# Optimization experiments

Measured on AMD Instinct MI355X. Metric: run time of the kernel, lower is better.

## Reference

```python
import jax, jax.numpy as jnp
import numpy as np

B, N, H, DK, DV = 2, 2048, 16, 128, 128
E = H * DV
EPS = 1e-6


def setup_inputs() -> dict:
    key = jax.random.key(0)
    ks = jax.random.split(key, 8)
    sc_qk = 1.0 / np.sqrt(E + H * DK)  # xavier_normal-ish std
    sc_e = 1.0 / np.sqrt(2 * E)
    d = {
        "x": jax.random.normal(ks[0], (B, N, E), jnp.float32),
        "Wq": jax.random.normal(ks[1], (H * DK, E), jnp.float32) * sc_qk,
        "bq": jnp.zeros((H * DK,), jnp.float32),
        "Wk": jax.random.normal(ks[2], (H * DK, E), jnp.float32) * sc_qk,
        "bk": jnp.zeros((H * DK,), jnp.float32),
        "Wv": jax.random.normal(ks[3], (E, E), jnp.float32) * sc_e,
        "bv": jnp.zeros((E,), jnp.float32),
        "Wg": jax.random.normal(ks[4], (E, E), jnp.float32) * sc_e,
        "bg": jnp.zeros((E,), jnp.float32),
        "Wo": jax.random.normal(ks[5], (E, E), jnp.float32) * sc_e,
        "bo": jnp.zeros((E,), jnp.float32),
        "start_idx": 0,
    }
    return d


def _retention_scan(q, k, v, decays):
    # q,k: [B,N,H,DK] (k already scaled), v: [B,N,H,DV]
    qs = jnp.moveaxis(q, 1, 0)  # [N,B,H,DK]
    ks_ = jnp.moveaxis(k, 1, 0)
    vs = jnp.moveaxis(v, 1, 0)
    dec = decays[None, :, None, None]  # [1,H,1,1]

    def step(state, qkv):
        qt, kt, vt = qkv
        # state_n = decay * state_{n-1} + k_n (x) v_n
        state = dec * state + kt[..., :, None] * vt[..., None, :]  # [B,H,DK,DV]
        ret = jnp.einsum("bhk,bhkv->bhv", qt, state)
        return state, ret

    init = jnp.zeros((q.shape[0], H, DK, DV), q.dtype)
    final_state, rets = jax.lax.scan(step, init, (qs, ks_, vs))
    return jnp.moveaxis(rets, 0, 1), final_state  # [B,N,H,DV], [B,H,DK,DV]


def reference(x, Wq, bq, Wk, bk, Wv, bv, Wg, bg, Wo, bo, start_idx):
    b, n, _ = x.shape
    decays = 1.0 - jnp.exp2(-5.0 - jnp.arange(H, dtype=jnp.float32))  # [H]
    q = (x @ Wq.T + bq).reshape(b, n, H, DK)
    k = (x @ Wk.T + bk).reshape(b, n, H, DK) / (DK ** 0.5)
    v = (x @ Wv.T + bv).reshape(b, n, H, DV)
    retention, state = _retention_scan(q, k, v, decays)
    # GroupNorm over (b n) tokens, num_groups=H, channels=E, no affine
    r = retention.reshape(b * n, H, DV).astype(jnp.float32)
    mu = jnp.mean(r, axis=-1, keepdims=True)
    var = jnp.var(r, axis=-1, keepdims=True)
    r = (r - mu) / jnp.sqrt(var + EPS)
    r = r.reshape(b, n, E).astype(x.dtype)
    gate = jax.nn.silu(x @ Wg.T + bg)
    out = (r * gate) @ Wo.T + bo
    return out, state
```

## Files before the change

kernel.cpp:

```cpp
#include <hip/hip_runtime.h>
#include <hip/hip_bf16.h>

typedef __attribute__((ext_vector_type(8))) short short8;
typedef __attribute__((ext_vector_type(4))) short short4v;
typedef __attribute__((ext_vector_type(4))) float floatx4;

#define DI __device__ __forceinline__

constexpr int B_ = 2, N_ = 2048, H_ = 16, DK_ = 128, DV_ = 128, E_ = 2048;
constexpr int M_ = B_ * N_;
constexpr int NCAT_ = 4 * E_;
constexpr int CH_ = 128;
constexpr int NC_ = N_ / CH_;
constexpr float KSCALE = 0.08838834764831845f;

constexpr long OFF_XB   = 0;
constexpr long OFF_WCAT = 16777216;
constexpr long OFF_WOB  = 50331648;
constexpr long OFF_BCAT = 58720256;
constexpr long OFF_Y    = 58753024;
constexpr long OFF_KT   = 125861888;
constexpr long OFF_VT   = 142639104;
constexpr long OFF_SCB  = 159416320;

DI unsigned short f2bf(float f){
  unsigned u = __float_as_uint(f);
  u += 0x7fffu + ((u >> 16) & 1u);
  return (unsigned short)(u >> 16);
}
DI float bf2f(unsigned short s){ return __uint_as_float(((unsigned)s) << 16); }

DI void gload_lds16(const void* g, void* l){
  __builtin_amdgcn_global_load_lds(
      (const __attribute__((address_space(1))) unsigned int*)g,
      (__attribute__((address_space(3))) unsigned int*)l, 16, 0, 0);
}

__global__ void k_cast(const float* __restrict__ s, unsigned short* __restrict__ d, int n){
  long i = ((long)blockIdx.x * blockDim.x + threadIdx.x) * 8;
  if(i >= n) return;
  float4 v0 = *(const float4*)(s + i);
  float4 v1 = *(const float4*)(s + i + 4);
  short8 o;
  o[0]=(short)f2bf(v0.x); o[1]=(short)f2bf(v0.y); o[2]=(short)f2bf(v0.z); o[3]=(short)f2bf(v0.w);
  o[4]=(short)f2bf(v1.x); o[5]=(short)f2bf(v1.y); o[6]=(short)f2bf(v1.z); o[7]=(short)f2bf(v1.w);
  *(short8*)(d + i) = o;
}

__global__ void k_bcat(const float* __restrict__ bq, const float* __restrict__ bk,
                       const float* __restrict__ bv, const float* __restrict__ bg,
                       float* __restrict__ bcat){
  int i = blockIdx.x * blockDim.x + threadIdx.x;
  float v;
  if(i < 2048)      v = bq[i];
  else if(i < 4096) v = bk[i - 2048];
  else if(i < 6144) v = bv[i - 4096];
  else              v = bg[i - 6144];
  bcat[i] = v;
}

__global__ __launch_bounds__(512, 2)
void k_gemm256(const unsigned short* __restrict__ A,
               const unsigned short* __restrict__ Bt,
               unsigned short* __restrict__ Y,
               const float* __restrict__ bias)
{
  extern __shared__ unsigned short lds[];
  constexpr int K = 2048;
  constexpr int NKT = K / 64;

  const int tid = threadIdx.x;
  const int wave = tid >> 6, lane = tid & 63;
  const int wr = wave >> 2, wc = wave & 3;
  const int l15 = lane & 15;

  int bid = blockIdx.x;
  int g = bid & 7, w = bid >> 3;
  int bm = (g & 1) * 8 + (w & 7);
  int bn = (g >> 1) * 8 + (w >> 3);

  const unsigned short* Ab = A  + (long)bm * 256 * K;
  const unsigned short* Bb = Bt + (long)bn * 256 * K;

  const int srow = wave * 8 + (lane >> 3);
  const int ce   = ((lane & 7) ^ ((lane >> 3) & 7)) * 8;

  const int colb[2] = { (((lane >> 4)    ) ^ (lane & 7)) << 4,
                        (((lane >> 4) + 4 ^ (lane & 7))) << 4 };
  int rbA[4], rbB[2];
  #pragma unroll
  for(int i=0;i<4;++i) rbA[i] = (wr*64 + i*16 + l15) << 7;
  #pragma unroll
  for(int j=0;j<2;++j) rbB[j] = (wc*32 + j*16 + l15) << 7;

  floatx4 acc[4][4][2] = {};
  short8 ar[4][2], br[2][2];
  const char* ldsc = (const char*)lds;

#define STG(op, buf, half, kt) do{                                                   \
    const unsigned short* _s = ((op) ? Bb : Ab) + (long)((half)*128 + srow)*K + (long)(kt)*64 + ce; \
    unsigned short* _d = lds + ((op)*32768 + (buf)*16384 + (half)*8192 + wave*512);  \
    gload_lds16(_s, _d);                                                             \
    gload_lds16(_s + 64*K, _d + 4096);                                               \
  }while(0)

#define RD_A(buf, half) do{                                                          \
    const char* _h = ldsc + (buf)*32768 + (half)*16384;                              \
    _Pragma("unroll")                                                                \
    for(int i=0;i<4;++i){ ar[i][0] = *(const short8*)(_h + rbA[i] + colb[0]);        \
                          ar[i][1] = *(const short8*)(_h + rbA[i] + colb[1]); }      \
  }while(0)

#define RD_B(buf, half) do{                                                          \
    const char* _h = ldsc + 65536 + (buf)*32768 + (half)*16384;                      \
    _Pragma("unroll")                                                                \
    for(int j=0;j<2;++j){ br[j][0] = *(const short8*)(_h + rbB[j] + colb[0]);        \
                          br[j][1] = *(const short8*)(_h + rbB[j] + colb[1]); }      \
  }while(0)

#define MFMA16(q) do{                                                                \
    __builtin_amdgcn_s_setprio(1);                                                   \
    _Pragma("unroll")                                                                \
    for(int i=0;i<4;++i)                                                             \
      _Pragma("unroll")                                                              \
      for(int j=0;j<2;++j)                                                           \
        _Pragma("unroll")                                                            \
        for(int k=0;k<2;++k)                                                         \
          acc[q][i][j] = __builtin_amdgcn_mfma_f32_16x16x32_bf16(ar[i][k], br[j][k], acc[q][i][j], 0,0,0); \
    __builtin_amdgcn_s_setprio(0);                                                   \
  }while(0)

  STG(0, 0, 0, 0);
  STG(1, 0, 0, 0);
  STG(1, 0, 1, 0);
  STG(0, 0, 1, 0);
  asm volatile("s_waitcnt vmcnt(0)" ::: "memory");
  __builtin_amdgcn_s_barrier();
  __builtin_amdgcn_sched_barrier(0);

  for(int u=0; u<NKT; ++u){
    const int cur = u & 1, nxt = cur ^ 1;
    const int ktn = (u + 1) & (NKT - 1);

    RD_A(cur, 0);
    RD_B(cur, 0);
    STG(0, nxt, 0, ktn);
    asm volatile("s_waitcnt vmcnt(4)" ::: "memory");
    __builtin_amdgcn_s_barrier();
    MFMA16(0);
    __builtin_amdgcn_s_barrier();
    __builtin_amdgcn_sched_barrier(0);

    RD_B(cur, 1);
    STG(1, nxt, 0, ktn);
    asm volatile("s_waitcnt vmcnt(4)" ::: "memory");
    __builtin_amdgcn_s_barrier();
    MFMA16(1);
    __builtin_amdgcn_s_barrier();
    __builtin_amdgcn_sched_barrier(0);

    RD_A(cur, 1);
    STG(1, nxt, 1, ktn);
    __builtin_amdgcn_s_barrier();
    MFMA16(2);
    __builtin_amdgcn_s_barrier();
    __builtin_amdgcn_sched_barrier(0);

    RD_B(cur, 0);
    STG(0, nxt, 1, ktn);
    asm volatile("s_waitcnt vmcnt(4)" ::: "memory");
    __builtin_amdgcn_s_barrier();
    MFMA16(3);
    __builtin_amdgcn_s_barrier();
    __builtin_amdgcn_sched_barrier(0);
  }
#undef STG
#undef RD_A
#undef RD_B
#undef MFMA16

  static constexpr int QM[4] = {0,0,1,1}, QN[4] = {0,1,1,0};
  #pragma unroll
  for(int q=0;q<4;++q){
    #pragma unroll
    for(int i=0;i<4;++i){
      const int rowi = bm*256 + QM[q]*128 + wr*64 + i*16 + ((lane>>4)<<2);
      #pragma unroll
      for(int j=0;j<2;++j){
        const int col = bn*256 + QN[q]*128 + wc*32 + j*16 + l15;
        const float bs = bias[col];
        const int sec = col >> 11;
        #pragma unroll
        for(int r=0;r<4;++r){
          float v = acc[q][i][j][r] + bs;
          if(sec == 1) v *= KSCALE;
          else if(sec == 3) v = v / (1.f + __expf(-v));
          Y[(long)(rowi + r) * NCAT_ + col] = f2bf(v);
        }
      }
    }
  }
}

template<int EPI>
__global__ __launch_bounds__(256)
void k_gemm(const unsigned short* __restrict__ A,
            const unsigned short* __restrict__ Bt,
            void* __restrict__ outp,
            const float* __restrict__ bias,
            int M, int Ncols, int K, int NB)
{
  __shared__ unsigned short lA[128*64];
  __shared__ unsigned short lB[128*64];
  const int bid = blockIdx.x;
  const int bm = bid / NB, bn = bid % NB;
  const int tid = threadIdx.x;
  const int wave = tid >> 6, lane = tid & 63;
  const int wr = wave >> 1, wc = wave & 1;

  floatx4 acc[4][4] = {};

  int srow[4], scol[4];
  #pragma unroll
  for(int is=0; is<4; ++is){
    int o = is*4096 + wave*1024 + lane*16;
    int row = o >> 7;
    int logcb = (o & 127) ^ ((row & 7) << 4);
    srow[is] = row; scol[is] = logcb >> 1;
  }
  const unsigned short* Abase = A + (long)bm * 128 * K;
  const unsigned short* Bbase = Bt + (long)bn * 128 * K;

  const int nkt = K >> 6;
  for(int kt=0; kt<nkt; ++kt){
    const int k0 = kt << 6;
    #pragma unroll
    for(int is=0; is<4; ++is){
      gload_lds16(Abase + (long)srow[is]*K + k0 + scol[is], &lA[(is*4096 + wave*1024) >> 1]);
      gload_lds16(Bbase + (long)srow[is]*K + k0 + scol[is], &lB[(is*4096 + wave*1024) >> 1]);
    }
    __syncthreads();
    #pragma unroll
    for(int kk=0; kk<2; ++kk){
      const int cb = (kk<<6) + ((lane>>4)<<4);
      short8 af[4], bfr[4];
      #pragma unroll
      for(int i=0;i<4;++i){
        int row = (wr<<6) + (i<<4) + (lane&15);
        af[i] = *(const short8*)((const char*)lA + (row<<7) + (cb ^ ((row&7)<<4)));
      }
      #pragma unroll
      for(int j=0;j<4;++j){
        int row = (wc<<6) + (j<<4) + (lane&15);
        bfr[j] = *(const short8*)((const char*)lB + (row<<7) + (cb ^ ((row&7)<<4)));
      }
      #pragma unroll
      for(int i=0;i<4;++i)
        #pragma unroll
        for(int j=0;j<4;++j)
          acc[i][j] = __builtin_amdgcn_mfma_f32_16x16x32_bf16(af[i], bfr[j], acc[i][j], 0,0,0);
    }
    __syncthreads();
  }

  #pragma unroll
  for(int i=0;i<4;++i){
    #pragma unroll
    for(int j=0;j<4;++j){
      #pragma unroll
      for(int r=0;r<4;++r){
        int row = bm*128 + (wr<<6) + (i<<4) + ((lane>>4)<<2) + r;
        int col = bn*128 + (wc<<6) + (j<<4) + (lane&15);
        float v = acc[i][j][r] + bias[col];
        if(EPI == 0){
          int sec = col >> 11;
          if(sec == 1) v *= KSCALE;
          else if(sec == 3) v = v / (1.f + __expf(-v));
          ((unsigned short*)outp)[(long)row * Ncols + col] = f2bf(v);
        } else {
          ((float*)outp)[(long)row * Ncols + col] = v;
        }
      }
    }
  }
}

__global__ __launch_bounds__(256)
void k_transpose(const unsigned short* __restrict__ Y,
                 unsigned short* __restrict__ Kt, unsigned short* __restrict__ Vt){
  __shared__ unsigned short lt[128][136];
  int bid = blockIdx.x;
  int op = bid >> 9;
  int r  = bid & 511;
  int bh = r >> 4, c = r & 15, b = bh >> 4, h = bh & 15;
  int tid = threadIdx.x;
  float dec = 1.f - exp2f(-5.f - (float)h);
  float l2d = log2f(dec);
  int sec = op ? 4096 : 2048;
  unsigned short* Dst = op ? Vt : Kt;

  #pragma unroll
  for(int p=0;p<8;++p){
    int t = p*16 + (tid>>4);
    long src = ((long)(b*N_ + c*CH_ + t)) * NCAT_ + sec + h*128 + (tid&15)*8;
    short8 v = *(const short8*)(Y + src);
    if(op == 0){
      float f = exp2f(-(float)t * l2d);
      #pragma unroll
      for(int u=0;u<8;++u) v[u] = (short)f2bf(bf2f((unsigned short)v[u]) * f);
    }
    *(short8*)&lt[t][(tid&15)*8] = v;
  }
  __syncthreads();
  #pragma unroll
  for(int p=0;p<8;++p){
    int dk = p*16 + (tid>>4);
    int tc = (tid&15)*8;
    short8 o;
    #pragma unroll
    for(int u=0;u<8;++u) o[u] = (short)lt[tc+u][dk];
    *(short8*)(Dst + ((long)(bh*128 + dk)) * N_ + c*CH_ + tc) = o;
  }
}

__global__ __launch_bounds__(256)
void k_chunksum(const unsigned short* __restrict__ Ktd, const unsigned short* __restrict__ Vt,
                float* __restrict__ MS){
  int bid = blockIdx.x;
  int bh = bid >> 4, c = bid & 15, h = bh & 15;
  int tid = threadIdx.x, wave = tid >> 6, lane = tid & 63;
  int wr = wave >> 1, wc = wave & 1;
  floatx4 acc[4][4] = {};
  const unsigned short* Vb = Vt  + (long)bh*128*N_ + c*CH_;
  const unsigned short* Kb = Ktd + (long)bh*128*N_ + c*CH_;

  #pragma unroll
  for(int kk=0;kk<4;++kk){
    int tl = kk*32 + ((lane>>4)<<3);
    short8 af[4], bfr[4];
    #pragma unroll
    for(int i=0;i<4;++i){ int dv = (wr<<6)+(i<<4)+(lane&15); af[i]  = *(const short8*)(Vb + (long)dv*N_ + tl); }
    #pragma unroll
    for(int j=0;j<4;++j){ int dk = (wc<<6)+(j<<4)+(lane&15); bfr[j] = *(const short8*)(Kb + (long)dk*N_ + tl); }
    #pragma unroll
    for(int i=0;i<4;++i)
      #pragma unroll
      for(int j=0;j<4;++j)
        acc[i][j] = __builtin_amdgcn_mfma_f32_16x16x32_bf16(af[i], bfr[j], acc[i][j], 0,0,0);
  }
  float dec = 1.f - exp2f(-5.f - (float)h);
  float scale = exp2f(127.f * log2f(dec));
  float* Mo = MS + ((long)bh*NC_ + c) * 16384;
  #pragma unroll
  for(int i=0;i<4;++i)
    #pragma unroll
    for(int j=0;j<4;++j)
      #pragma unroll
      for(int r=0;r<4;++r){
        int dv = (wr<<6)+(i<<4)+((lane>>4)<<2)+r;
        int dk = (wc<<6)+(j<<4)+(lane&15);
        Mo[dv*128 + dk] = acc[i][j][r] * scale;
      }
}

__global__ __launch_bounds__(256)
void k_scan(const float* __restrict__ MS, unsigned short* __restrict__ Scb,
            float* __restrict__ stateOut){
  int bid = blockIdx.x;
  int bh = bid >> 4, p = bid & 15;
  int tid = threadIdx.x, h = bh & 15;
  float dec = 1.f - exp2f(-5.f - (float)h);
  float decC = exp2f(128.f * log2f(dec));
  int e0 = p*1024 + tid*4;
  floatx4 S = {0.f, 0.f, 0.f, 0.f};
  const float* base = MS + (long)bh * NC_ * 16384 + e0;
  unsigned short* sb = Scb + (long)bh * NC_ * 16384 + e0;
  for(int c=0;c<NC_;++c){
    floatx4 m = *(const floatx4*)(base + (long)c*16384);
    short4v q;
    #pragma unroll
    for(int u=0;u<4;++u) q[u] = (short)f2bf(S[u]);
    *(short4v*)(sb + (long)c*16384) = q;
    S = decC * S + m;
  }
  int dv = e0 >> 7, dk = e0 & 127;
  float* so = stateOut + (long)bh*16384 + dv;
  #pragma unroll
  for(int u=0;u<4;++u) so[(long)(dk+u)*128] = S[u];
}

__global__ __launch_bounds__(256)
void k_ret(const unsigned short* __restrict__ Y, const unsigned short* __restrict__ Vt,
           const unsigned short* __restrict__ Scb, unsigned short* __restrict__ RG){
  __shared__ unsigned short sQ[128*128];
  __shared__ unsigned short sK[128*128];
  int bid = blockIdx.x;
  int bh = bid >> 4, c = bid & 15, b = bh >> 4, h = bh & 15;
  int tid = threadIdx.x, w = tid >> 6, lane = tid & 63;
  float dec = 1.f - exp2f(-5.f - (float)h);
  float l2d = log2f(dec);

  #pragma unroll
  for(int p=0;p<8;++p){
    int t = p*16 + (tid>>4);
    long row = (long)(b*N_ + c*CH_ + t) * NCAT_ + h*128 + (tid&15)*8;
    short8 qv = *(const short8*)(Y + row);
    short8 kv = *(const short8*)(Y + row + 2048);
    float fq = exp2f((float)t * l2d);
    float fk = exp2f(-(float)t * l2d);
    short8 qs, ks;
    #pragma unroll
    for(int u=0;u<8;++u){
      qs[u] = (short)f2bf(bf2f((unsigned short)qv[u]) * fq);
      ks[u] = (short)f2bf(bf2f((unsigned short)kv[u]) * fk);
    }
    int ad = t*256 + (((tid&15)*16) ^ ((t&7)<<4));
    *(short8*)((char*)sQ + ad) = qs;
    *(short8*)((char*)sK + ad) = ks;
  }
  __syncthreads();

  floatx4 acc[2][8] = {};
  #pragma unroll
  for(int kk=0;kk<4;++kk){
    int cb = (kk<<6) + ((lane>>4)<<4);
    short8 af[2], bfr[8];
    #pragma unroll
    for(int i=0;i<2;++i){ int t = w*32 + (i<<4) + (lane&15); af[i] = *(const short8*)((const char*)sQ + t*256 + (cb ^ ((t&7)<<4))); }
    #pragma unroll
    for(int j=0;j<8;++j){ int s = (j<<4) + (lane&15); bfr[j] = *(const short8*)((const char*)sK + s*256 + (cb ^ ((s&7)<<4))); }
    #pragma unroll
    for(int i=0;i<2;++i)
      #pragma unroll
      for(int j=0;j<8;++j)
        acc[i][j] = __builtin_amdgcn_mfma_f32_16x16x32_bf16(af[i], bfr[j], acc[i][j], 0,0,0);
  }
  __syncthreads();

  #pragma unroll
  for(int i=0;i<2;++i)
    #pragma unroll
    for(int j=0;j<8;++j)
      #pragma unroll
      for(int r=0;r<4;++r){
        int t = w*32 + (i<<4) + ((lane>>4)<<2) + r;
        int s = (j<<4) + (lane&15);
        float v = (s <= t) ? acc[i][j][r] : 0.f;
        *(unsigned short*)((char*)sK + t*256 + ((s*2) ^ ((t&7)<<4))) = f2bf(v);
      }
  __syncthreads();

  #pragma unroll
  for(int i=0;i<2;++i)
    #pragma unroll
    for(int j=0;j<8;++j)
      #pragma unroll
      for(int u=0;u<4;++u) acc[i][j][u] = 0.f;

  const unsigned short* Vb = Vt + (long)bh*128*N_ + c*CH_;
  #pragma unroll
  for(int kk=0;kk<4;++kk){
    int cb = (kk<<6) + ((lane>>4)<<4);
    int sg = kk*32 + ((lane>>4)<<3);
    short8 af[2], bfr[8];
    #pragma unroll
    for(int i=0;i<2;++i){ int t = w*32 + (i<<4) + (lane&15); af[i] = *(const short8*)((const char*)sK + t*256 + (cb ^ ((t&7)<<4))); }
    #pragma unroll
    for(int j=0;j<8;++j){ int dv = (j<<4) + (lane&15); bfr[j] = *(const short8*)(Vb + (long)dv*N_ + sg); }
    #pragma unroll
    for(int i=0;i<2;++i)
      #pragma unroll
      for(int j=0;j<8;++j)
        acc[i][j] = __builtin_amdgcn_mfma_f32_16x16x32_bf16(af[i], bfr[j], acc[i][j], 0,0,0);
  }
  const unsigned short* Sb = Scb + ((long)bh*NC_ + c) * 16384;
  #pragma unroll
  for(int kk=0;kk<4;++kk){
    int cb = (kk<<6) + ((lane>>4)<<4);
    int kg = kk*32 + ((lane>>4)<<3);
    short8 af[2], bfr[8];
    #pragma unroll
    for(int i=0;i<2;++i){
      int t = w*32 + (i<<4) + (lane&15);
      short8 qv = *(const short8*)((const char*)sQ + t*256 + (cb ^ ((t&7)<<4)));
      #pragma unroll
      for(int u=0;u<8;++u) af[i][u] = (short)f2bf(bf2f((unsigned short)qv[u]) * dec);
    }
    #pragma unroll
    for(int j=0;j<8;++j){ int dv = (j<<4) + (lane&15); bfr[j] = *(const short8*)(Sb + (long)dv*128 + kg); }
    #pragma unroll
    for(int i=0;i<2;++i)
      #pragma unroll
      for(int j=0;j<8;++j)
        acc[i][j] = __builtin_amdgcn_mfma_f32_16x16x32_bf16(af[i], bfr[j], acc[i][j], 0,0,0);
  }

  #pragma unroll
  for(int i=0;i<2;++i){
    #pragma unroll
    for(int r=0;r<4;++r){
      float s1 = 0.f, s2 = 0.f;
      #pragma unroll
      for(int j=0;j<8;++j){ float v = acc[i][j][r]; s1 += v; s2 += v*v; }
      #pragma unroll
      for(int off=1; off<16; off<<=1){ s1 += __shfl_xor(s1, off); s2 += __shfl_xor(s2, off); }
      float mu  = s1 * (1.f/128.f);
      float var = s2 * (1.f/128.f) - mu*mu;
      float inv = rsqrtf(var + 1e-6f);
      int t = w*32 + (i<<4) + ((lane>>4)<<2) + r;
      long mrow = (long)(b*N_ + c*CH_ + t);
      #pragma unroll
      for(int j=0;j<8;++j){
        int dv = (j<<4) + (lane&15);
        float v = (acc[i][j][r] - mu) * inv;
        float g = bf2f(Y[mrow*NCAT_ + 6144 + h*128 + dv]);
        RG[mrow*E_ + h*128 + dv] = f2bf(v * g);
      }
    }
  }
}

extern "C" void kernel_launch(void* const* d_in, const int* in_sizes, int n_in,
                              void* d_out, int out_size, void* d_ws, size_t ws_size,
                              hipStream_t stream) {
  const float* x  = (const float*)d_in[0];
  const float* Wq = (const float*)d_in[1];
  const float* bq = (const float*)d_in[2];
  const float* Wk = (const float*)d_in[3];
  const float* bk = (const float*)d_in[4];
  const float* Wv = (const float*)d_in[5];
  const float* bv = (const float*)d_in[6];
  const float* Wg = (const float*)d_in[7];
  const float* bg = (const float*)d_in[8];
  const float* Wo = (const float*)d_in[9];
  const float* bo = (const float*)d_in[10];

  char* ws = (char*)d_ws;
  unsigned short* xb   = (unsigned short*)(ws + OFF_XB);
  unsigned short* Wcat = (unsigned short*)(ws + OFF_WCAT);
  unsigned short* Wob  = (unsigned short*)(ws + OFF_WOB);
  float*          bcat = (float*)(ws + OFF_BCAT);
  unsigned short* Y    = (unsigned short*)(ws + OFF_Y);
  unsigned short* Ktd  = (unsigned short*)(ws + OFF_KT);
  unsigned short* Vt   = (unsigned short*)(ws + OFF_VT);
  unsigned short* Scb  = (unsigned short*)(ws + OFF_SCB);
  float*          MS   = (float*)(ws + OFF_WCAT);
  unsigned short* RG   = (unsigned short*)(ws + OFF_XB);

  float* outp     = (float*)d_out;
  float* stateOut = outp + (long)M_ * E_;

  (void)hipFuncSetAttribute((const void*)k_gemm256,
                            hipFuncAttributeMaxDynamicSharedMemorySize, 131072);

  k_cast<<<4096, 256, 0, stream>>>(x, xb, M_*E_);
  k_cast<<<2048, 256, 0, stream>>>(Wq, Wcat + 0L,        E_*E_);
  k_cast<<<2048, 256, 0, stream>>>(Wk, Wcat + 1L*E_*E_,  E_*E_);
  k_cast<<<2048, 256, 0, stream>>>(Wv, Wcat + 2L*E_*E_,  E_*E_);
  k_cast<<<2048, 256, 0, stream>>>(Wg, Wcat + 3L*E_*E_,  E_*E_);
  k_cast<<<2048, 256, 0, stream>>>(Wo, Wob, E_*E_);
  k_bcat<<<32, 256, 0, stream>>>(bq, bk, bv, bg, bcat);

  k_gemm256<<<512, 512, 131072, stream>>>(xb, Wcat, Y, bcat);

  k_transpose<<<1024, 256, 0, stream>>>(Y, Ktd, Vt);

  k_chunksum<<<512, 256, 0, stream>>>(Ktd, Vt, MS);
  k_scan<<<512, 256, 0, stream>>>(MS, Scb, stateOut);
  k_ret<<<512, 256, 0, stream>>>(Y, Vt, Scb, RG);

  k_gemm<1><<<(M_/128)*(E_/128), 256, 0, stream>>>(RG, Wob, (void*)outp, bo, M_, E_, E_, E_/128);
}
```

Before: 295.3 us.

## Simplify fused projection GEMM pipeline and double-buffer the output GEMM

The 256x256-tile projection GEMM drops its hand-scheduled four-phase loop, which used partial vmcnt waits, barriers and priority hints. In its place is a plain double-buffered loop: one __syncthreads, prefetch of the next K-tile into the other buffer, then two k-steps of 8x4 MFMAs over the whole tile. The 128x128 output GEMM gets a second LDS buffer so the next tile's global-to-LDS loads overlap the current tile's MFMAs, which also removes one barrier per iteration. The trade is simpler code and more overlap in the small GEMM, at the risk of less fine-grained memory/compute interleaving in the large GEMM. The doubled LDS use in the small GEMM may also lower occupancy.

```diff
diff --git a/kernel.cpp b/kernel.cpp
--- a/kernel.cpp
+++ b/kernel.cpp
@@ -85,16 +85,15 @@
   const int srow = wave * 8 + (lane >> 3);
   const int ce   = ((lane & 7) ^ ((lane >> 3) & 7)) * 8;
 
-  const int colb[2] = { (((lane >> 4)    ) ^ (lane & 7)) << 4,
-                        (((lane >> 4) + 4 ^ (lane & 7))) << 4 };
-  int rbA[4], rbB[2];
-  #pragma unroll
-  for(int i=0;i<4;++i) rbA[i] = (wr*64 + i*16 + l15) << 7;
-  #pragma unroll
-  for(int j=0;j<2;++j) rbB[j] = (wc*32 + j*16 + l15) << 7;
-
-  floatx4 acc[4][4][2] = {};
-  short8 ar[4][2], br[2][2];
+  const int colb[2] = { ((((lane >> 4))    ^ (lane & 7)) << 4),
+                        ((((lane >> 4)+4)  ^ (lane & 7)) << 4) };
+  int rbA[8], rbB[4];
+  #pragma unroll
+  for(int ai=0;ai<8;++ai) rbA[ai] = (ai>>2)*16384 + ((wr*64 + (ai&3)*16 + l15) << 7);
+  #pragma unroll
+  for(int bj=0;bj<4;++bj) rbB[bj] = (bj>>1)*16384 + ((wc*32 + (bj&1)*16 + l15) << 7);
+
+  floatx4 acc[8][4] = {};
   const char* ldsc = (const char*)lds;
 
 #define STG(op, buf, half, kt) do{                                                   \
@@ -104,99 +103,55 @@
     gload_lds16(_s + 64*K, _d + 4096);                                               \
   }while(0)
 
-#define RD_A(buf, half) do{                                                          \
-    const char* _h = ldsc + (buf)*32768 + (half)*16384;                              \
-    _Pragma("unroll")                                                                \
-    for(int i=0;i<4;++i){ ar[i][0] = *(const short8*)(_h + rbA[i] + colb[0]);        \
-                          ar[i][1] = *(const short8*)(_h + rbA[i] + colb[1]); }      \
-  }while(0)
-
-#define RD_B(buf, half) do{                                                          \
-    const char* _h = ldsc + 65536 + (buf)*32768 + (half)*16384;                      \
-    _Pragma("unroll")                                                                \
-    for(int j=0;j<2;++j){ br[j][0] = *(const short8*)(_h + rbB[j] + colb[0]);        \
-                          br[j][1] = *(const short8*)(_h + rbB[j] + colb[1]); }      \
-  }while(0)
-
-#define MFMA16(q) do{                                                                \
-    __builtin_amdgcn_s_setprio(1);                                                   \
-    _Pragma("unroll")                                                                \
-    for(int i=0;i<4;++i)                                                             \
-      _Pragma("unroll")                                                              \
-      for(int j=0;j<2;++j)                                                           \
-        _Pragma("unroll")                                                            \
-        for(int k=0;k<2;++k)                                                         \
-          acc[q][i][j] = __builtin_amdgcn_mfma_f32_16x16x32_bf16(ar[i][k], br[j][k], acc[q][i][j], 0,0,0); \
-    __builtin_amdgcn_s_setprio(0);                                                   \
-  }while(0)
-
   STG(0, 0, 0, 0);
   STG(1, 0, 0, 0);
+  STG(0, 0, 1, 0);
   STG(1, 0, 1, 0);
-  STG(0, 0, 1, 0);
-  asm volatile("s_waitcnt vmcnt(0)" ::: "memory");
-  __builtin_amdgcn_s_barrier();
-  __builtin_amdgcn_sched_barrier(0);
 
   for(int u=0; u<NKT; ++u){
     const int cur = u & 1, nxt = cur ^ 1;
     const int ktn = (u + 1) & (NKT - 1);
 
-    RD_A(cur, 0);
-    RD_B(cur, 0);
+    __syncthreads();
+
     STG(0, nxt, 0, ktn);
-    asm volatile("s_waitcnt vmcnt(4)" ::: "memory");
-    __builtin_amdgcn_s_barrier();
-    MFMA16(0);
-    __builtin_amdgcn_s_barrier();
-    __builtin_amdgcn_sched_barrier(0);
-
-    RD_B(cur, 1);
     STG(1, nxt, 0, ktn);
-    asm volatile("s_waitcnt vmcnt(4)" ::: "memory");
-    __builtin_amdgcn_s_barrier();
-    MFMA16(1);
-    __builtin_amdgcn_s_barrier();
-    __builtin_amdgcn_sched_barrier(0);
-
-    RD_A(cur, 1);
+    STG(0, nxt, 1, ktn);
     STG(1, nxt, 1, ktn);
-    __builtin_amdgcn_s_barrier();
-    MFMA16(2);
-    __builtin_amdgcn_s_barrier();
-    __builtin_amdgcn_sched_barrier(0);
-
-    RD_B(cur, 0);
-    STG(0, nxt, 1, ktn);
-    asm volatile("s_waitcnt vmcnt(4)" ::: "memory");
-    __builtin_amdgcn_s_barrier();
-    MFMA16(3);
-    __builtin_amdgcn_s_barrier();
-    __builtin_amdgcn_sched_barrier(0);
+
+    const char* cA = ldsc + cur*32768;
+    const char* cB = ldsc + 65536 + cur*32768;
+
+    #pragma unroll
+    for(int kk=0;kk<2;++kk){
+      short8 a8[8], b4[4];
+      #pragma unroll
+      for(int ai=0;ai<8;++ai) a8[ai] = *(const short8*)(cA + rbA[ai] + colb[kk]);
+      #pragma unroll
+      for(int bj=0;bj<4;++bj) b4[bj] = *(const short8*)(cB + rbB[bj] + colb[kk]);
+      #pragma unroll
+      for(int ai=0;ai<8;++ai)
+        #pragma unroll
+        for(int bj=0;bj<4;++bj)
+          acc[ai][bj] = __builtin_amdgcn_mfma_f32_16x16x32_bf16(a8[ai], b4[bj], acc[ai][bj], 0,0,0);
+    }
   }
 #undef STG
-#undef RD_A
-#undef RD_B
-#undef MFMA16
-
-  static constexpr int QM[4] = {0,0,1,1}, QN[4] = {0,1,1,0};
-  #pragma unroll
-  for(int q=0;q<4;++q){
-    #pragma unroll
-    for(int i=0;i<4;++i){
-      const int rowi = bm*256 + QM[q]*128 + wr*64 + i*16 + ((lane>>4)<<2);
-      #pragma unroll
-      for(int j=0;j<2;++j){
-        const int col = bn*256 + QN[q]*128 + wc*32 + j*16 + l15;
-        const float bs = bias[col];
-        const int sec = col >> 11;
-        #pragma unroll
-        for(int r=0;r<4;++r){
-          float v = acc[q][i][j][r] + bs;
-          if(sec == 1) v *= KSCALE;
-          else if(sec == 3) v = v / (1.f + __expf(-v));
-          Y[(long)(rowi + r) * NCAT_ + col] = f2bf(v);
-        }
+
+  #pragma unroll
+  for(int ai=0;ai<8;++ai){
+    const int rowi = bm*256 + (ai>>2)*128 + wr*64 + (ai&3)*16 + ((lane>>4)<<2);
+    #pragma unroll
+    for(int bj=0;bj<4;++bj){
+      const int col = bn*256 + (bj>>1)*128 + wc*32 + (bj&1)*16 + l15;
+      const float bs = bias[col];
+      const int sec = col >> 11;
+      #pragma unroll
+      for(int r=0;r<4;++r){
+        float v = acc[ai][bj][r] + bs;
+        if(sec == 1) v *= KSCALE;
+        else if(sec == 3) v = v / (1.f + __expf(-v));
+        Y[(long)(rowi + r) * NCAT_ + col] = f2bf(v);
       }
     }
   }
@@ -210,8 +165,8 @@
             const float* __restrict__ bias,
             int M, int Ncols, int K, int NB)
 {
-  __shared__ unsigned short lA[128*64];
-  __shared__ unsigned short lB[128*64];
+  __shared__ unsigned short lA[2*128*64];
+  __shared__ unsigned short lB[2*128*64];
   const int bid = blockIdx.x;
   const int bm = bid / NB, bn = bid % NB;
   const int tid = threadIdx.x;
@@ -231,15 +186,24 @@
   const unsigned short* Abase = A + (long)bm * 128 * K;
   const unsigned short* Bbase = Bt + (long)bn * 128 * K;
 
+#define STG128(kt, buf) do{                                                          \
+    const int _k0 = (kt) << 6;                                                       \
+    _Pragma("unroll")                                                                \
+    for(int is=0; is<4; ++is){                                                       \
+      gload_lds16(Abase + (long)srow[is]*K + _k0 + scol[is], &lA[(buf)*8192 + ((is*4096 + wave*1024) >> 1)]); \
+      gload_lds16(Bbase + (long)srow[is]*K + _k0 + scol[is], &lB[(buf)*8192 + ((is*4096 + wave*1024) >> 1)]); \
+    }                                                                                \
+  }while(0)
+
   const int nkt = K >> 6;
+  STG128(0, 0);
   for(int kt=0; kt<nkt; ++kt){
-    const int k0 = kt << 6;
-    #pragma unroll
-    for(int is=0; is<4; ++is){
-      gload_lds16(Abase + (long)srow[is]*K + k0 + scol[is], &lA[(is*4096 + wave*1024) >> 1]);
-      gload_lds16(Bbase + (long)srow[is]*K + k0 + scol[is], &lB[(is*4096 + wave*1024) >> 1]);
-    }
+    const int cur = kt & 1, nxt = cur ^ 1;
+    const int ktn = (kt + 1 == nkt) ? 0 : kt + 1;
     __syncthreads();
+    STG128(ktn, nxt);
+    const char* cA = (const char*)lA + cur*16384;
+    const char* cB = (const char*)lB + cur*16384;
     #pragma unroll
     for(int kk=0; kk<2; ++kk){
       const int cb = (kk<<6) + ((lane>>4)<<4);
@@ -247,12 +211,12 @@
       #pragma unroll
       for(int i=0;i<4;++i){
         int row = (wr<<6) + (i<<4) + (lane&15);
-        af[i] = *(const short8*)((const char*)lA + (row<<7) + (cb ^ ((row&7)<<4)));
+        af[i] = *(const short8*)(cA + (row<<7) + (cb ^ ((row&7)<<4)));
       }
       #pragma unroll
       for(int j=0;j<4;++j){
         int row = (wc<<6) + (j<<4) + (lane&15);
-        bfr[j] = *(const short8*)((const char*)lB + (row<<7) + (cb ^ ((row&7)<<4)));
+        bfr[j] = *(const short8*)(cB + (row<<7) + (cb ^ ((row&7)<<4)));
       }
       #pragma unroll
       for(int i=0;i<4;++i)
@@ -260,8 +224,8 @@
         for(int j=0;j<4;++j)
           acc[i][j] = __builtin_amdgcn_mfma_f32_16x16x32_bf16(af[i], bfr[j], acc[i][j], 0,0,0);
     }
-    __syncthreads();
-  }
+  }
+#undef STG128
 
   #pragma unroll
   for(int i=0;i<4;++i){
```

New measurement: 295.8 us. About the same (+0.2%).
